# Kernel optimization log

Hardware: AMD Instinct MI355X
Metric: run time of the kernel (lower is better)

Reference implementation:

```python
import jax, jax.numpy as jnp
import numpy as np

jax.config.update("jax_enable_x64", True)

P = 2013265921          # NTT-friendly prime 15 * 2**27 + 1 (int64-safe proxy for BLS12-377 Fr)
GEN = 31                # generator of the multiplicative group of F_P
LOGN = 22
N = 1 << LOGN           # domain_size
C = 4                   # columns, as in the module docstring example


def _pow_table(base, n):
    """powers[k] = base**k mod P for k in [0, n), built by repeated doubling (vectorized)."""
    pw = np.ones(n, dtype=np.int64)
    cur = base % P
    step = 1
    while step < n:
        hi = min(2 * step, n)
        pw[step:hi] = (pw[:hi - step] * cur) % P
        cur = (cur * cur) % P
        step *= 2
    return pw


def setup_inputs() -> dict:
    key = jax.random.key(0)
    x = jax.random.randint(key, (N, C), 0, P, dtype=jnp.int64)
    omega = pow(GEN, (P - 1) // N, P)          # primitive N-th root of unity
    omega_inv = pow(omega, P - 2, P)           # its inverse (Fermat)
    twiddles = jnp.asarray(_pow_table(omega_inv, N // 2))  # omega_inv**k, k < N/2  (the 'Params' table)
    n_inv = jnp.asarray(pow(N, P - 2, P), dtype=jnp.int64)  # N^{-1} mod P
    return {"input": x, "twiddles": twiddles, "n_inv": n_inv}


def reference(input, twiddles, n_inv):
    """Inverse NTT over F_P, columns transformed independently. Output in natural order."""
    n, c = input.shape
    logn = n.bit_length() - 1
    # bit-reversal permutation indices (static; computed with numpy)
    idx = np.arange(n)
    rev = np.zeros(n, dtype=np.int64)
    for i in range(logn):
        rev = (rev << 1) | ((idx >> i) & 1)
    x = input[rev]
    # iterative Cooley-Tukey butterflies, logn stages
    for s in range(1, logn + 1):
        m = 1 << s
        half = m >> 1
        w = twiddles[:: n // m]                 # [half] = omega_inv**(j * n/m)
        xr = x.reshape(-1, m, c)                # [n/m, m, c]
        lo, hi = xr[:, :half], xr[:, half:]
        t = (w[None, :, None] * hi) % P         # modular twiddle multiply
        x = jnp.concatenate([(lo + t) % P, (lo - t) % P], axis=1).reshape(n, c)
    return (x * n_inv) % P                      # scale by N^{-1}
```

## Files before the change

kernel.cpp:

```cpp
#include <hip/hip_runtime.h>
#include <stdint.h>

static constexpr uint32_t P = 2013265921u;
static constexpr int      LOGM = 11;
static constexpr int      MSZ  = 1 << LOGM;

__host__ __device__ constexpr uint32_t neg_pinv32() {
    uint32_t x = 1u;
    for (int i = 0; i < 5; ++i) x *= 2u - P * x;
    return 0u - x;
}
static constexpr uint32_t NEG_PINV = neg_pinv32();
static constexpr uint32_t R1 = (uint32_t)(((uint64_t)1 << 32) % P);
static constexpr uint32_t R2 = (uint32_t)(((uint64_t)R1 * R1) % P);

__device__ __forceinline__ uint32_t mont_mul(uint32_t a, uint32_t b) {
    uint64_t t = (uint64_t)a * (uint64_t)b;
    uint32_t m = (uint32_t)t * NEG_PINV;
    uint32_t r = (uint32_t)((t + (uint64_t)m * P) >> 32);
    uint32_t s = r - P;
    return s < r ? s : r;
}
__device__ __forceinline__ uint32_t to_mont(uint32_t a) { return mont_mul(a, R2); }
__device__ __forceinline__ uint32_t add_p(uint32_t a, uint32_t b) {
    uint32_t r = a + b, s = r - P; return s < r ? s : r;
}
__device__ __forceinline__ uint32_t sub_p(uint32_t a, uint32_t b) {
    uint32_t r = a - b, s = r + P; return s < r ? s : r;
}

__device__ __forceinline__ uint4 mm4(uint32_t w, uint4 v) {
    return make_uint4(mont_mul(w, v.x), mont_mul(w, v.y),
                      mont_mul(w, v.z), mont_mul(w, v.w));
}
__device__ __forceinline__ void bf4(uint4& L, uint4& H, uint32_t w) {
    uint4 t = mm4(w, H);
    uint4 l = L;
    L = make_uint4(add_p(l.x, t.x), add_p(l.y, t.y), add_p(l.z, t.z), add_p(l.w, t.w));
    H = make_uint4(sub_p(l.x, t.x), sub_p(l.y, t.y), sub_p(l.z, t.z), sub_p(l.w, t.w));
}

__device__ __forceinline__ int fmap(int i) {
    return i ^ (((i >> 3) ^ (i >> 6)) & 7);
}

__device__ __forceinline__ void radix8(uint4 x[8],
        uint32_t ta, uint32_t tb0, uint32_t tb1,
        uint32_t tc0, uint32_t tc1, uint32_t tc2, uint32_t tc3) {
    bf4(x[0], x[1], ta);  bf4(x[2], x[3], ta);
    bf4(x[4], x[5], ta);  bf4(x[6], x[7], ta);
    bf4(x[0], x[2], tb0); bf4(x[1], x[3], tb1);
    bf4(x[4], x[6], tb0); bf4(x[5], x[7], tb1);
    bf4(x[0], x[4], tc0); bf4(x[1], x[5], tc1);
    bf4(x[2], x[6], tc2); bf4(x[3], x[7], tc3);
}

template <bool PASS2>
__global__ __launch_bounds__(256, 4) void intt_pass(
        const uint4* __restrict__ src, uint4* __restrict__ dst,
        const uint32_t* __restrict__ tw,
        const uint32_t* __restrict__ ninv_p)
{
    __shared__ uint4    buf[MSZ];
    __shared__ uint32_t rtab[MSZ / 2];

    const int      tid = threadIdx.x;
    const uint32_t bid = blockIdx.x;
    const uint32_t col = ((bid & 7u) << 8) | (bid >> 3);

    uint32_t tv[4];
#pragma unroll
    for (int j = 0; j < 4; ++j)
        tv[j] = tw[(uint32_t)(tid + 256 * j) << LOGM];

    const uint32_t r8 = __brev((uint32_t)tid) >> 24;
    uint4 x[8];
#pragma unroll
    for (int m = 0; m < 8; ++m) {
        uint32_t r3 = __brev((uint32_t)m) >> 29;
        x[m] = src[((r3 << 8) | r8) * (uint32_t)MSZ + col];
    }
#pragma unroll
    for (int j = 0; j < 4; ++j)
        rtab[tid + 256 * j] = to_mont(tv[j]);
    __syncthreads();

    radix8(x, rtab[0], rtab[0], rtab[512],
              rtab[0], rtab[256], rtab[512], rtab[768]);
#pragma unroll
    for (int m = 0; m < 8; ++m) buf[fmap(8 * tid + m)] = x[m];
    __syncthreads();

    {
        const int L = tid & 7, hi = tid >> 3;
        const int base = (hi << 6) | L;
#pragma unroll
        for (int m = 0; m < 8; ++m) x[m] = buf[fmap(base | (m << 3))];
        radix8(x, rtab[L << 7],
                  rtab[L << 6], rtab[(L << 6) + 512],
                  rtab[L << 5], rtab[(L << 5) + 256],
                  rtab[(L << 5) + 512], rtab[(L << 5) + 768]);
#pragma unroll
        for (int m = 0; m < 8; ++m) buf[fmap(base | (m << 3))] = x[m];
    }
    __syncthreads();

    {
        const int L = tid & 63, hi = tid >> 6;
        const int base = (hi << 9) | L;
#pragma unroll
        for (int m = 0; m < 8; ++m) x[m] = buf[fmap(base | (m << 6))];
        radix8(x, rtab[L << 4],
                  rtab[L << 3], rtab[(L << 3) + 512],
                  rtab[L << 2], rtab[(L << 2) + 256],
                  rtab[(L << 2) + 512], rtab[(L << 2) + 768]);
#pragma unroll
        for (int m = 0; m < 8; ++m) buf[fmap(base | (m << 6))] = x[m];
    }
    __syncthreads();

    const uint32_t nm   = PASS2 ? to_mont(*ninv_p) : 0u;
    const uint32_t step = PASS2 ? 0u : to_mont(tw[col << 9]);
#pragma unroll
    for (int g = 0; g < 2; ++g) {
        const int lo = tid + (g << 8);
        uint4 y[4];
#pragma unroll
        for (int m = 0; m < 4; ++m) y[m] = buf[fmap(lo | (m << 9))];
        const uint32_t t10  = rtab[lo << 1];
        const uint32_t t110 = rtab[lo];
        const uint32_t t111 = rtab[lo + 512];
        bf4(y[0], y[1], t10);  bf4(y[2], y[3], t10);
        bf4(y[0], y[2], t110); bf4(y[1], y[3], t111);

        if (!PASS2) {
            uint32_t tm = to_mont(tw[col * (uint32_t)lo]);
#pragma unroll
            for (int m = 0; m < 4; ++m) {
                dst[col * (uint32_t)MSZ + (uint32_t)((m << 9) | lo)] = mm4(tm, y[m]);
                tm = mont_mul(tm, step);
            }
        } else {
#pragma unroll
            for (int m = 0; m < 4; ++m)
                dst[(uint32_t)((m << 9) | lo) * (uint32_t)MSZ + col] = mm4(nm, y[m]);
        }
    }
}

extern "C" void kernel_launch(void* const* d_in, const int* in_sizes, int n_in,
                              void* d_out, int out_size, void* d_ws, size_t ws_size,
                              hipStream_t stream)
{
    const uint4*    x    = (const uint4*)d_in[0];
    const uint32_t* tw   = (const uint32_t*)d_in[1];
    const uint32_t* ninv = (const uint32_t*)d_in[2];
    uint4*          out  = (uint4*)d_out;

    intt_pass<false><<<dim3(2048), dim3(256), 0, stream>>>(x, out, tw, ninv);
    intt_pass<true ><<<dim3(2048), dim3(256), 0, stream>>>(out, out, tw, ninv);
}
```

Before: 216.5 us.

## Process four adjacent columns per block with interleaved LDS and stage-ordered twiddle table

Each block now handles four neighbouring sub-transform columns with 1024 threads, where the low two thread bits pick the column. Global loads of the strided pass then cover 64 contiguous bytes per row instead of 16, which should improve coalescing. The twiddle table is rebuilt in a stage-major layout so each stage reads contiguous entries, and the per-element twist factor is carried forward by repeated multiplication instead of a strided global gather. The cost is 128KB of LDS per block, which limits occupancy to roughly one block per CU, and fewer blocks overall.

```diff
diff --git a/kernel.cpp b/kernel.cpp
--- a/kernel.cpp
+++ b/kernel.cpp
@@ -4,6 +4,7 @@
 static constexpr uint32_t P = 2013265921u;
 static constexpr int      LOGM = 11;
 static constexpr int      MSZ  = 1 << LOGM;
+static constexpr int      NCOL = 4;
 
 __host__ __device__ constexpr uint32_t neg_pinv32() {
     uint32_t x = 1u;
@@ -28,7 +29,6 @@
 __device__ __forceinline__ uint32_t sub_p(uint32_t a, uint32_t b) {
     uint32_t r = a - b, s = r + P; return s < r ? s : r;
 }
-
 __device__ __forceinline__ uint4 mm4(uint32_t w, uint4 v) {
     return make_uint4(mont_mul(w, v.x), mont_mul(w, v.y),
                       mont_mul(w, v.z), mont_mul(w, v.w));
@@ -40,9 +40,10 @@
     H = make_uint4(sub_p(l.x, t.x), sub_p(l.y, t.y), sub_p(l.z, t.z), sub_p(l.w, t.w));
 }
 
-__device__ __forceinline__ int fmap(int i) {
-    return i ^ (((i >> 3) ^ (i >> 6)) & 7);
+__device__ __forceinline__ int g_sw(int el) {
+    return el ^ (((el >> 3) ^ (el >> 6)) & 7);
 }
+__device__ __forceinline__ int fidx(int el, int c) { return (g_sw(el) << 2) | c; }
 
 __device__ __forceinline__ void radix8(uint4 x[8],
         uint32_t ta, uint32_t tb0, uint32_t tb1,
@@ -56,94 +57,102 @@
 }
 
 template <bool PASS2>
-__global__ __launch_bounds__(256, 4) void intt_pass(
+__global__ __launch_bounds__(1024, 4) void intt_pass(
         const uint4* __restrict__ src, uint4* __restrict__ dst,
         const uint32_t* __restrict__ tw,
         const uint32_t* __restrict__ ninv_p)
 {
-    __shared__ uint4    buf[MSZ];
-    __shared__ uint32_t rtab[MSZ / 2];
+    __shared__ uint4    buf[MSZ * NCOL];
+    __shared__ uint32_t stab[2048];
 
-    const int      tid = threadIdx.x;
+    const int      t   = threadIdx.x;
+    const int      c4  = t & 3;
+    const int      sub = t >> 2;
     const uint32_t bid = blockIdx.x;
-    const uint32_t col = ((bid & 7u) << 8) | (bid >> 3);
+    const uint32_t grp = ((bid & 7u) << 6) | (bid >> 3);
+    const uint32_t c   = (grp << 2) | (uint32_t)c4;
 
-    uint32_t tv[4];
 #pragma unroll
-    for (int j = 0; j < 4; ++j)
-        tv[j] = tw[(uint32_t)(tid + 256 * j) << LOGM];
+    for (int q = 0; q < 2; ++q) {
+        int e = 2 * t + q;
+        if (e < 2047) {
+            uint32_t ep1 = (uint32_t)e + 1u;
+            int sm1 = 31 - __clz((int)ep1);
+            uint32_t j = ep1 - (1u << sm1);
+            stab[e] = to_mont(tw[j << (21 - sm1)]);
+        }
+    }
 
-    const uint32_t r8 = __brev((uint32_t)tid) >> 24;
+    const uint32_t r8 = __brev((uint32_t)sub) >> 24;
     uint4 x[8];
 #pragma unroll
     for (int m = 0; m < 8; ++m) {
         uint32_t r3 = __brev((uint32_t)m) >> 29;
-        x[m] = src[((r3 << 8) | r8) * (uint32_t)MSZ + col];
+        x[m] = src[((r3 << 8) | r8) * (uint32_t)MSZ + c];
     }
-#pragma unroll
-    for (int j = 0; j < 4; ++j)
-        rtab[tid + 256 * j] = to_mont(tv[j]);
     __syncthreads();
 
-    radix8(x, rtab[0], rtab[0], rtab[512],
-              rtab[0], rtab[256], rtab[512], rtab[768]);
+    radix8(x, stab[0], stab[1], stab[2], stab[3], stab[4], stab[5], stab[6]);
 #pragma unroll
-    for (int m = 0; m < 8; ++m) buf[fmap(8 * tid + m)] = x[m];
+    for (int m = 0; m < 8; ++m) buf[fidx(8 * sub + m, c4)] = x[m];
     __syncthreads();
 
     {
-        const int L = tid & 7, hi = tid >> 3;
+        const int L = sub & 7, hi = sub >> 3;
         const int base = (hi << 6) | L;
 #pragma unroll
-        for (int m = 0; m < 8; ++m) x[m] = buf[fmap(base | (m << 3))];
-        radix8(x, rtab[L << 7],
-                  rtab[L << 6], rtab[(L << 6) + 512],
-                  rtab[L << 5], rtab[(L << 5) + 256],
-                  rtab[(L << 5) + 512], rtab[(L << 5) + 768]);
+        for (int m = 0; m < 8; ++m) x[m] = buf[fidx(base | (m << 3), c4)];
+        radix8(x, stab[7 + L], stab[15 + L], stab[23 + L],
+                  stab[31 + L], stab[39 + L], stab[47 + L], stab[55 + L]);
 #pragma unroll
-        for (int m = 0; m < 8; ++m) buf[fmap(base | (m << 3))] = x[m];
+        for (int m = 0; m < 8; ++m) buf[fidx(base | (m << 3), c4)] = x[m];
     }
     __syncthreads();
 
     {
-        const int L = tid & 63, hi = tid >> 6;
+        const int L = sub & 63, hi = sub >> 6;
         const int base = (hi << 9) | L;
 #pragma unroll
-        for (int m = 0; m < 8; ++m) x[m] = buf[fmap(base | (m << 6))];
-        radix8(x, rtab[L << 4],
-                  rtab[L << 3], rtab[(L << 3) + 512],
-                  rtab[L << 2], rtab[(L << 2) + 256],
-                  rtab[(L << 2) + 512], rtab[(L << 2) + 768]);
+        for (int m = 0; m < 8; ++m) x[m] = buf[fidx(base | (m << 6), c4)];
+        radix8(x, stab[63 + L], stab[127 + L], stab[191 + L],
+                  stab[255 + L], stab[319 + L], stab[383 + L], stab[447 + L]);
 #pragma unroll
-        for (int m = 0; m < 8; ++m) buf[fmap(base | (m << 6))] = x[m];
+        for (int m = 0; m < 8; ++m) buf[fidx(base | (m << 6), c4)] = x[m];
     }
     __syncthreads();
 
-    const uint32_t nm   = PASS2 ? to_mont(*ninv_p) : 0u;
-    const uint32_t step = PASS2 ? 0u : to_mont(tw[col << 9]);
+    uint32_t nm = 0u, s256 = 0u, step512 = 0u, tm0 = 0u;
+    if (PASS2) {
+        nm = to_mont(*ninv_p);
+    } else {
+        s256    = to_mont(tw[c << 8]);
+        step512 = mont_mul(s256, s256);
+        tm0     = to_mont(tw[c * (uint32_t)sub]);
+    }
 #pragma unroll
-    for (int g = 0; g < 2; ++g) {
-        const int lo = tid + (g << 8);
+    for (int gg = 0; gg < 2; ++gg) {
+        const int lo = sub + (gg << 8);
         uint4 y[4];
 #pragma unroll
-        for (int m = 0; m < 4; ++m) y[m] = buf[fmap(lo | (m << 9))];
-        const uint32_t t10  = rtab[lo << 1];
-        const uint32_t t110 = rtab[lo];
-        const uint32_t t111 = rtab[lo + 512];
+        for (int m = 0; m < 4; ++m) y[m] = buf[fidx(lo | (m << 9), c4)];
+        const uint32_t t10  = stab[511 + lo];
+        const uint32_t t110 = stab[1023 + lo];
+        const uint32_t t111 = stab[1535 + lo];
         bf4(y[0], y[1], t10);  bf4(y[2], y[3], t10);
         bf4(y[0], y[2], t110); bf4(y[1], y[3], t111);
 
         if (!PASS2) {
-            uint32_t tm = to_mont(tw[col * (uint32_t)lo]);
+            uint32_t tm = tm0;
 #pragma unroll
             for (int m = 0; m < 4; ++m) {
-                dst[col * (uint32_t)MSZ + (uint32_t)((m << 9) | lo)] = mm4(tm, y[m]);
-                tm = mont_mul(tm, step);
+                dst[c * (uint32_t)MSZ + (uint32_t)((m << 9) | lo)] = mm4(tm, y[m]);
+                tm = mont_mul(tm, step512);
             }
+            tm0 = mont_mul(tm0, s256);
         } else {
 #pragma unroll
             for (int m = 0; m < 4; ++m)
-                dst[(uint32_t)((m << 9) | lo) * (uint32_t)MSZ + col] = mm4(nm, y[m]);
+                dst[(uint32_t)((m << 9) | lo) * (uint32_t)MSZ + c] = mm4(nm, y[m]);
         }
     }
 }
@@ -157,6 +166,6 @@
     const uint32_t* ninv = (const uint32_t*)d_in[2];
     uint4*          out  = (uint4*)d_out;
 
-    intt_pass<false><<<dim3(2048), dim3(256), 0, stream>>>(x, out, tw, ninv);
-    intt_pass<true ><<<dim3(2048), dim3(256), 0, stream>>>(out, out, tw, ninv);
+    intt_pass<false><<<dim3(512), dim3(1024), 0, stream>>>(x, out, tw, ninv);
+    intt_pass<true ><<<dim3(512), dim3(1024), 0, stream>>>(out, out, tw, ninv);
 }
```

Result: faster. 209.6 us (-3.2%).
